# Performance work log

Measured on AMD Instinct MI355X. Metric: run time of the kernel, lower is better.

The kernel has to match this reference:

```python
import jax, jax.numpy as jnp
import numpy as np

S, B, C = 7, 2, 20
LAMBDA_COORD, LAMBDA_NOOBJ = 5.0, 0.5
N, T = 16384, 32


def setup_inputs() -> dict:
    key = jax.random.key(0)
    k1, k2, k3 = jax.random.split(key, 3)
    outputs = jax.random.normal(k1, (N, S, S, B * 5 + C), dtype=jnp.float32)
    # center-format normalized boxes [x, y, w, h] in (0, 1)
    target_boxes = jax.random.uniform(k2, (N, T, 4), dtype=jnp.float32)
    target_labels = jax.random.randint(k3, (N, T), 0, C, dtype=jnp.int32)
    return {"outputs": outputs, "target_boxes": target_boxes, "target_labels": target_labels}


def _iou(b1, b2):
    # center-format boxes [..., 4] -> IoU, broadcasting over leading dims
    x11, y11 = b1[..., 0] - b1[..., 2] / 2, b1[..., 1] - b1[..., 3] / 2
    x12, y12 = b1[..., 0] + b1[..., 2] / 2, b1[..., 1] + b1[..., 3] / 2
    x21, y21 = b2[..., 0] - b2[..., 2] / 2, b2[..., 1] - b2[..., 3] / 2
    x22, y22 = b2[..., 0] + b2[..., 2] / 2, b2[..., 1] + b2[..., 3] / 2
    iw = jnp.clip(jnp.minimum(x12, x22) - jnp.maximum(x11, x21), 0.0)
    ih = jnp.clip(jnp.minimum(y12, y22) - jnp.maximum(y11, y21), 0.0)
    inter = iw * ih
    union = b1[..., 2] * b1[..., 3] + b2[..., 2] * b2[..., 3] - inter
    return inter / jnp.maximum(union, 1e-6)


def yolo_v1_loss(outputs, target_boxes, target_labels):
    n = outputs.shape[0]
    pred_boxes = outputs[..., : B * 4].reshape(n, S, S, B, 4)  # [n,S,S,B,4]
    pred_conf = outputs[..., B * 4 : B * 5]                    # [n,S,S,B]
    pred_cls = outputs[..., B * 5 :]                           # [n,S,S,C]

    cell = 1.0 / S
    g = jnp.arange(S, dtype=jnp.float32)
    px = (pred_boxes[..., 0] + g[None, None, :, None]) * cell  # grid_x varies along dim 2
    py = (pred_boxes[..., 1] + g[None, :, None, None]) * cell  # grid_y varies along dim 1
    pred_boxes_g = jnp.stack([px, py, pred_boxes[..., 2], pred_boxes[..., 3]], axis=-1)

    tx, ty, tw, th = (target_boxes[..., i] for i in range(4))
    gxi = jnp.clip((tx / cell).astype(jnp.int32), 0, S - 1)   # [n,T]
    gyi = jnp.clip((ty / cell).astype(jnp.int32), 0, S - 1)
    ox = (tx - gxi.astype(jnp.float32) * cell) / cell
    oy = (ty - gyi.astype(jnp.float32) * cell) / cell

    bidx = jnp.arange(n)[:, None]
    cell_boxes = pred_boxes_g[bidx, gyi, gxi]  # [n,T,B,4]
    cell_conf = pred_conf[bidx, gyi, gxi]      # [n,T,B]
    cell_cls = pred_cls[bidx, gyi, gxi]        # [n,T,C]

    ious = _iou(target_boxes[:, :, None, :], cell_boxes)          # [n,T,B]
    best = jnp.argmax(ious, axis=-1)                              # [n,T]
    best_box = jnp.take_along_axis(cell_boxes, best[..., None, None], axis=2)[:, :, 0]  # [n,T,4]
    best_conf = jnp.take_along_axis(cell_conf, best[..., None], axis=2)[:, :, 0]        # [n,T]

    pw = jnp.maximum(best_box[..., 2], 1e-6)
    ph = jnp.maximum(best_box[..., 3], 1e-6)
    twc = jnp.maximum(tw, 1e-6)
    thc = jnp.maximum(th, 1e-6)
    box_loss = (
        (best_box[..., 0] - ox) ** 2
        + (best_box[..., 1] - oy) ** 2
        + (jnp.sqrt(pw) - jnp.sqrt(twc)) ** 2
        + (jnp.sqrt(ph) - jnp.sqrt(thc)) ** 2
    ).sum(axis=1)                                                # per-image sum over targets

    obj_loss = ((best_conf - 1.0) ** 2).sum(axis=1)

    onehot = jax.nn.one_hot(target_labels, C, dtype=jnp.float32)
    class_loss = jnp.mean((jax.nn.softmax(cell_cls, axis=-1) - onehot) ** 2, axis=-1).sum(axis=1)

    # obj_mask is never set in the original, so noobj covers every cell/box
    noobj_loss = jnp.mean(pred_conf ** 2, axis=(1, 2, 3))

    per_img = LAMBDA_COORD * box_loss + class_loss + obj_loss + LAMBDA_NOOBJ * noobj_loss
    return jnp.mean(per_img)


def reference(outputs, target_boxes, target_labels):
    return yolo_v1_loss(outputs, target_boxes, target_labels)
```

## Files before the change

kernel.cpp:

```cpp
#include <hip/hip_runtime.h>
#include <math.h>

#define TPB 256
constexpr int kS = 7;
constexpr int kB = 2;
constexpr int kC = 20;
constexpr int kT = 32;
constexpr int kCH = kB * 5 + kC;
constexpr int kCells = kS * kS;
constexpr int kImgF = kCells * kCH;
constexpr int IMGS = 8;

__device__ __forceinline__ float block_reduce(float v, float* red) {
    #pragma unroll
    for (int off = 32; off > 0; off >>= 1)
        v += __shfl_down(v, off, 64);
    const int lane = threadIdx.x & 63;
    const int wave = threadIdx.x >> 6;
    if (lane == 0) red[wave] = v;
    __syncthreads();
    float s = 0.0f;
    if (threadIdx.x == 0) {
        #pragma unroll
        for (int w = 0; w < TPB / 64; w++) s += red[w];
    }
    return s;
}

__global__ __launch_bounds__(TPB) void yolo_stage1(
    const float* __restrict__ outputs,
    const float4* __restrict__ tboxes,
    const int* __restrict__ tlabels,
    float* __restrict__ blocksums,
    int n)
{
    __shared__ float red[TPB / 64];
    const int tid = threadIdx.x;
    const int img0 = blockIdx.x * IMGS;
    const int nimg = min(IMGS, n - img0);

    float local = 0.0f;
    const float kno = 0.5f / (float)(2 * kCells);

    const bool has_tgt = tid < nimg * kT;
    float4 tb = make_float4(0.f, 0.f, 0.f, 0.f);
    int lab = 0;
    if (has_tgt) {
        tb = tboxes[(size_t)img0 * kT + tid];
        lab = tlabels[(size_t)img0 * kT + tid];
    }

    if (nimg == IMGS) {
        const float4* src = reinterpret_cast<const float4*>(outputs + (size_t)img0 * kImgF);
        constexpr int NV4 = IMGS * kImgF / 4;
        constexpr int FULL = NV4 / TPB;
        int base = (4 * tid) % 30;
        #pragma unroll
        for (int i = 0; i < FULL; i++) {
            const float4 v = src[tid + i * TPB];
            if (base == 8)      local += kno * (v.x * v.x + v.y * v.y);
            else if (base == 6) local += kno * (v.z * v.z + v.w * v.w);
            base += 4; if (base >= 30) base -= 30;
        }
        const int idx = tid + FULL * TPB;
        if (idx < NV4) {
            const float4 v = src[idx];
            if (base == 8)      local += kno * (v.x * v.x + v.y * v.y);
            else if (base == 6) local += kno * (v.z * v.z + v.w * v.w);
        }
    } else {
        const float* srcf = outputs + (size_t)img0 * kImgF;
        const int tot = nimg * kImgF;
        for (int i = tid; i < tot; i += TPB) {
            const float v = srcf[i];
            const int ch = i % kCH;
            if (ch == 8 || ch == 9) local += kno * v * v;
        }
    }

    if (has_tgt) {
        const int sub = tid >> 5;
        const float cellf = 1.0f / 7.0f;
        const float tx = tb.x, ty = tb.y, tw = tb.z, th = tb.w;

        int gxi = (int)(tx / cellf); gxi = min(max(gxi, 0), kS - 1);
        int gyi = (int)(ty / cellf); gyi = min(max(gyi, 0), kS - 1);
        const float ox = (tx - (float)gxi * cellf) / cellf;
        const float oy = (ty - (float)gyi * cellf) / cellf;
        const float* __restrict__ cellp =
            outputs + (size_t)(img0 + sub) * kImgF + (gyi * kS + gxi) * kCH;

        const float t_x1 = tx - tw * 0.5f, t_x2 = tx + tw * 0.5f;
        const float t_y1 = ty - th * 0.5f, t_y2 = ty + th * 0.5f;
        const float tarea = tw * th;
        float ious[2], bxs[2], bys[2], bws[2], bhs[2];
        #pragma unroll
        for (int b = 0; b < 2; b++) {
            const float x = cellp[4 * b + 0], y = cellp[4 * b + 1];
            const float w = cellp[4 * b + 2], h = cellp[4 * b + 3];
            const float px = (x + (float)gxi) * cellf;
            const float py = (y + (float)gyi) * cellf;
            const float x21 = px - w * 0.5f, x22 = px + w * 0.5f;
            const float y21 = py - h * 0.5f, y22 = py + h * 0.5f;
            const float iw = fmaxf(fminf(t_x2, x22) - fmaxf(t_x1, x21), 0.0f);
            const float ih = fmaxf(fminf(t_y2, y22) - fmaxf(t_y1, y21), 0.0f);
            const float inter = iw * ih;
            const float uni = tarea + w * h - inter;
            ious[b] = inter / fmaxf(uni, 1e-6f);
            bxs[b] = px; bys[b] = py; bws[b] = w; bhs[b] = h;
        }
        const int best = (ious[1] > ious[0]) ? 1 : 0;

        const float pw = fmaxf(bws[best], 1e-6f), ph = fmaxf(bhs[best], 1e-6f);
        const float twc = fmaxf(tw, 1e-6f), thc = fmaxf(th, 1e-6f);
        const float dx = bxs[best] - ox, dy = bys[best] - oy;
        const float dw = sqrtf(pw) - sqrtf(twc), dh = sqrtf(ph) - sqrtf(thc);
        const float box_loss = dx * dx + dy * dy + dw * dw + dh * dh;

        const float dconf = cellp[8 + best] - 1.0f;
        const float obj_loss = dconf * dconf;

        float cls[kC];
        #pragma unroll
        for (int c = 0; c < kC; c++) cls[c] = cellp[10 + c];
        float m = cls[0];
        #pragma unroll
        for (int c = 1; c < kC; c++) m = fmaxf(m, cls[c]);
        float ssum = 0.0f;
        #pragma unroll
        for (int c = 0; c < kC; c++) { cls[c] = __expf(cls[c] - m); ssum += cls[c]; }
        const float inv = 1.0f / ssum;
        float cl = 0.0f;
        #pragma unroll
        for (int c = 0; c < kC; c++) {
            const float d = cls[c] * inv - (c == lab ? 1.0f : 0.0f);
            cl += d * d;
        }

        local += 5.0f * box_loss + obj_loss + cl * (1.0f / (float)kC);
    }

    const float bsum = block_reduce(local, red);
    if (tid == 0) blocksums[blockIdx.x] = bsum;
}

__global__ __launch_bounds__(TPB) void yolo_stage2(
    const float* __restrict__ blocksums, int nblocks, float invn,
    float* __restrict__ out)
{
    __shared__ float red[TPB / 64];
    float local = 0.0f;
    for (int i = threadIdx.x; i < nblocks; i += TPB) local += blocksums[i];
    const float s = block_reduce(local, red);
    if (threadIdx.x == 0) out[0] = s * invn;
}

extern "C" void kernel_launch(void* const* d_in, const int* in_sizes, int n_in,
                              void* d_out, int out_size, void* d_ws, size_t ws_size,
                              hipStream_t stream)
{
    const float* outputs = (const float*)d_in[0];
    const float4* tboxes = (const float4*)d_in[1];
    const int* tlabels = (const int*)d_in[2];
    float* out = (float*)d_out;
    float* blocksums = (float*)d_ws;

    const int n = in_sizes[0] / kImgF;
    const int nblocks = (n + IMGS - 1) / IMGS;

    yolo_stage1<<<nblocks, TPB, 0, stream>>>(outputs, tboxes, tlabels, blocksums, n);
    yolo_stage2<<<1, TPB, 0, stream>>>(blocksums, nblocks, 1.0f / (float)n, out);
}
```

Measured before the change: 163.2 us.

## Split each target across two lanes and batch the noobj loads up front

Halves the images per block to 4 and assigns two threads to each target. Each lane handles one predicted box and half of the class logits, and the IoU, max and sum are exchanged through xor shuffles. All float4 loads for the noobj sum are issued before any accumulation, so more memory requests are in flight at once. Together these aim to cut per-thread gather latency and register pressure and to double the block count. In exchange the code adds shuffle overhead and uses smaller blocks.

```diff
diff --git a/kernel.cpp b/kernel.cpp
--- a/kernel.cpp
+++ b/kernel.cpp
@@ -9,7 +9,7 @@
 constexpr int kCH = kB * 5 + kC;
 constexpr int kCells = kS * kS;
 constexpr int kImgF = kCells * kCH;
-constexpr int IMGS = 8;
+constexpr int IMGS = 4;
 
 __device__ __forceinline__ float block_reduce(float v, float* red) {
     #pragma unroll
@@ -42,31 +42,39 @@
     float local = 0.0f;
     const float kno = 0.5f / (float)(2 * kCells);
 
-    const bool has_tgt = tid < nimg * kT;
+    const int pair = tid >> 1;
+    const int b = tid & 1;
+    const bool has_tgt = pair < nimg * kT;
     float4 tb = make_float4(0.f, 0.f, 0.f, 0.f);
     int lab = 0;
     if (has_tgt) {
-        tb = tboxes[(size_t)img0 * kT + tid];
-        lab = tlabels[(size_t)img0 * kT + tid];
+        tb = tboxes[(size_t)img0 * kT + pair];
+        lab = tlabels[(size_t)img0 * kT + pair];
     }
 
     if (nimg == IMGS) {
         const float4* src = reinterpret_cast<const float4*>(outputs + (size_t)img0 * kImgF);
         constexpr int NV4 = IMGS * kImgF / 4;
         constexpr int FULL = NV4 / TPB;
+        float4 vv[FULL];
+        #pragma unroll
+        for (int i = 0; i < FULL; i++) vv[i] = src[tid + i * TPB];
+        const int tidx = tid + FULL * TPB;
+        float4 vt = make_float4(0.f, 0.f, 0.f, 0.f);
+        const bool tok = tidx < NV4;
+        if (tok) vt = src[tidx];
+
         int base = (4 * tid) % 30;
         #pragma unroll
         for (int i = 0; i < FULL; i++) {
-            const float4 v = src[tid + i * TPB];
+            const float4 v = vv[i];
             if (base == 8)      local += kno * (v.x * v.x + v.y * v.y);
             else if (base == 6) local += kno * (v.z * v.z + v.w * v.w);
             base += 4; if (base >= 30) base -= 30;
         }
-        const int idx = tid + FULL * TPB;
-        if (idx < NV4) {
-            const float4 v = src[idx];
-            if (base == 8)      local += kno * (v.x * v.x + v.y * v.y);
-            else if (base == 6) local += kno * (v.z * v.z + v.w * v.w);
+        if (tok) {
+            if (base == 8)      local += kno * (vt.x * vt.x + vt.y * vt.y);
+            else if (base == 6) local += kno * (vt.z * vt.z + vt.w * vt.w);
         }
     } else {
         const float* srcf = outputs + (size_t)img0 * kImgF;
@@ -79,7 +87,7 @@
     }
 
     if (has_tgt) {
-        const int sub = tid >> 5;
+        const int sub = pair >> 5;
         const float cellf = 1.0f / 7.0f;
         const float tx = tb.x, ty = tb.y, tw = tb.z, th = tb.w;
 
@@ -87,57 +95,62 @@
         int gyi = (int)(ty / cellf); gyi = min(max(gyi, 0), kS - 1);
         const float ox = (tx - (float)gxi * cellf) / cellf;
         const float oy = (ty - (float)gyi * cellf) / cellf;
-        const float* __restrict__ cellp =
-            outputs + (size_t)(img0 + sub) * kImgF + (gyi * kS + gxi) * kCH;
+        const float2* __restrict__ cell2 = reinterpret_cast<const float2*>(
+            outputs + (size_t)(img0 + sub) * kImgF + (gyi * kS + gxi) * kCH);
+
+        const float2 xy = cell2[2 * b + 0];
+        const float2 wh = cell2[2 * b + 1];
+        const float2 cf = cell2[4];
+        float cls[10];
+        #pragma unroll
+        for (int j = 0; j < 5; j++) {
+            const float2 c2 = cell2[5 + 5 * b + j];
+            cls[2 * j] = c2.x; cls[2 * j + 1] = c2.y;
+        }
 
         const float t_x1 = tx - tw * 0.5f, t_x2 = tx + tw * 0.5f;
         const float t_y1 = ty - th * 0.5f, t_y2 = ty + th * 0.5f;
-        const float tarea = tw * th;
-        float ious[2], bxs[2], bys[2], bws[2], bhs[2];
+        const float px = (xy.x + (float)gxi) * cellf;
+        const float py = (xy.y + (float)gyi) * cellf;
+        const float x21 = px - wh.x * 0.5f, x22 = px + wh.x * 0.5f;
+        const float y21 = py - wh.y * 0.5f, y22 = py + wh.y * 0.5f;
+        const float iw = fmaxf(fminf(t_x2, x22) - fmaxf(t_x1, x21), 0.0f);
+        const float ih = fmaxf(fminf(t_y2, y22) - fmaxf(t_y1, y21), 0.0f);
+        const float inter = iw * ih;
+        const float uni = tw * th + wh.x * wh.y - inter;
+        const float iou_mine = inter / fmaxf(uni, 1e-6f);
+        const float iou_other = __shfl_xor(iou_mine, 1, 64);
+        const float iou0 = b ? iou_other : iou_mine;
+        const float iou1 = b ? iou_mine : iou_other;
+        const int best = (iou1 > iou0) ? 1 : 0;
+
+        if (b == best) {
+            const float pw = fmaxf(wh.x, 1e-6f), ph = fmaxf(wh.y, 1e-6f);
+            const float twc = fmaxf(tw, 1e-6f), thc = fmaxf(th, 1e-6f);
+            const float dx = px - ox, dy = py - oy;
+            const float dws = sqrtf(pw) - sqrtf(twc), dhs = sqrtf(ph) - sqrtf(thc);
+            const float box_loss = dx * dx + dy * dy + dws * dws + dhs * dhs;
+            const float dconf = (b ? cf.y : cf.x) - 1.0f;
+            local += 5.0f * box_loss + dconf * dconf;
+        }
+
+        float mh = cls[0];
         #pragma unroll
-        for (int b = 0; b < 2; b++) {
-            const float x = cellp[4 * b + 0], y = cellp[4 * b + 1];
-            const float w = cellp[4 * b + 2], h = cellp[4 * b + 3];
-            const float px = (x + (float)gxi) * cellf;
-            const float py = (y + (float)gyi) * cellf;
-            const float x21 = px - w * 0.5f, x22 = px + w * 0.5f;
-            const float y21 = py - h * 0.5f, y22 = py + h * 0.5f;
-            const float iw = fmaxf(fminf(t_x2, x22) - fmaxf(t_x1, x21), 0.0f);
-            const float ih = fmaxf(fminf(t_y2, y22) - fmaxf(t_y1, y21), 0.0f);
-            const float inter = iw * ih;
-            const float uni = tarea + w * h - inter;
-            ious[b] = inter / fmaxf(uni, 1e-6f);
-            bxs[b] = px; bys[b] = py; bws[b] = w; bhs[b] = h;
-        }
-        const int best = (ious[1] > ious[0]) ? 1 : 0;
-
-        const float pw = fmaxf(bws[best], 1e-6f), ph = fmaxf(bhs[best], 1e-6f);
-        const float twc = fmaxf(tw, 1e-6f), thc = fmaxf(th, 1e-6f);
-        const float dx = bxs[best] - ox, dy = bys[best] - oy;
-        const float dw = sqrtf(pw) - sqrtf(twc), dh = sqrtf(ph) - sqrtf(thc);
-        const float box_loss = dx * dx + dy * dy + dw * dw + dh * dh;
-
-        const float dconf = cellp[8 + best] - 1.0f;
-        const float obj_loss = dconf * dconf;
-
-        float cls[kC];
+        for (int j = 1; j < 10; j++) mh = fmaxf(mh, cls[j]);
+        const float m = fmaxf(mh, __shfl_xor(mh, 1, 64));
+        float sh = 0.0f;
         #pragma unroll
-        for (int c = 0; c < kC; c++) cls[c] = cellp[10 + c];
-        float m = cls[0];
-        #pragma unroll
-        for (int c = 1; c < kC; c++) m = fmaxf(m, cls[c]);
-        float ssum = 0.0f;
-        #pragma unroll
-        for (int c = 0; c < kC; c++) { cls[c] = __expf(cls[c] - m); ssum += cls[c]; }
+        for (int j = 0; j < 10; j++) { cls[j] = __expf(cls[j] - m); sh += cls[j]; }
+        const float ssum = sh + __shfl_xor(sh, 1, 64);
         const float inv = 1.0f / ssum;
         float cl = 0.0f;
+        const int labh = lab - 10 * b;
         #pragma unroll
-        for (int c = 0; c < kC; c++) {
-            const float d = cls[c] * inv - (c == lab ? 1.0f : 0.0f);
+        for (int j = 0; j < 10; j++) {
+            const float d = cls[j] * inv - (j == labh ? 1.0f : 0.0f);
             cl += d * d;
         }
-
-        local += 5.0f * box_loss + obj_loss + cl * (1.0f / (float)kC);
+        local += cl * (1.0f / (float)kC);
     }
 
     const float bsum = block_reduce(local, red);
```

Result: faster. 153.9 us, median of 2 (-5.7%).
